# Kernel optimization log

Measured on AMD Instinct MI355X. Metric: run time of the kernel, lower is better.

## Reference

```python
import jax, jax.numpy as jnp
import numpy as np

H = 256        # hidden_dim
GD = 16        # genome_dim
GL = 16        # genome_len
L = 2          # n_layers
NH = 4         # n_heads
ED = 256       # embed_dim (of generated network)
CS = 256       # chunk_size (== H so chunk feedback into GRU is well-formed)
TOTAL = 4 * ED * ED + 4 * ED          # 263168
NCH = (TOTAL + CS - 1) // CS          # 1028 sequential GRU steps
B = 16


def setup_inputs() -> dict:
    key = jax.random.key(0)
    ks = iter(jax.random.split(key, 32))
    def p(shape, s=0.02):
        return jax.random.normal(next(ks), shape, jnp.float32) * s
    return dict(
        genome_seq=jax.random.normal(next(ks), (B, GL, GD), jnp.float32),
        embed_W=p((H, GD)), embed_b=jnp.zeros((H,), jnp.float32),
        qkv_W=p((L, 3 * H, H)), qkv_b=jnp.zeros((L, 3 * H), jnp.float32),
        attn_out_W=p((L, H, H)), attn_out_b=jnp.zeros((L, H), jnp.float32),
        ln1_g=jnp.ones((L, H), jnp.float32), ln1_b=jnp.zeros((L, H), jnp.float32),
        ln2_g=jnp.ones((L, H), jnp.float32), ln2_b=jnp.zeros((L, H), jnp.float32),
        ffn_W1=p((L, 4 * H, H)), ffn_b1=jnp.zeros((L, 4 * H), jnp.float32),
        ffn_W2=p((L, H, 4 * H)), ffn_b2=jnp.zeros((L, H), jnp.float32),
        gru_Wih=p((3 * H, H)), gru_Whh=p((3 * H, H)),
        gru_bih=jnp.zeros((3 * H,), jnp.float32), gru_bhh=jnp.zeros((3 * H,), jnp.float32),
        out_W=p((CS, H)), out_b=jnp.zeros((CS,), jnp.float32),
    )


def _ln(x, g, b, eps=1e-5):
    m = x.mean(-1, keepdims=True)
    v = ((x - m) ** 2).mean(-1, keepdims=True)
    return (x - m) / jnp.sqrt(v + eps) * g + b


def reference(genome_seq, embed_W, embed_b, qkv_W, qkv_b, attn_out_W, attn_out_b,
              ln1_g, ln1_b, ln2_g, ln2_b, ffn_W1, ffn_b1, ffn_W2, ffn_b2,
              gru_Wih, gru_Whh, gru_bih, gru_bhh, out_W, out_b):
    b = genome_seq.shape[0]
    dh = H // NH
    scale = 1.0 / np.sqrt(dh).astype(np.float32)

    h = genome_seq @ embed_W.T + embed_b                      # [B, S, H]
    # post-norm transformer encoder, relu FFN (PyTorch defaults, no dropout)
    for l in range(L):
        qkv = h @ qkv_W[l].T + qkv_b[l]                        # [B, S, 3H]
        q, k, v = jnp.split(qkv, 3, axis=-1)
        q = q.reshape(b, GL, NH, dh)
        k = k.reshape(b, GL, NH, dh)
        v = v.reshape(b, GL, NH, dh)
        scores = jnp.einsum('bshd,bthd->bhst', q, k) * scale
        attn = jax.nn.softmax(scores, axis=-1)
        o = jnp.einsum('bhst,bthd->bshd', attn, v).reshape(b, GL, H)
        h = _ln(h + o @ attn_out_W[l].T + attn_out_b[l], ln1_g[l], ln1_b[l])
        f = jax.nn.relu(h @ ffn_W1[l].T + ffn_b1[l]) @ ffn_W2[l].T + ffn_b2[l]
        h = _ln(h + f, ln2_g[l], ln2_b[l])

    latent = h.mean(axis=1)                                    # [B, H]

    # sequential chunk generation: 1 GRU step + Linear per chunk, fed back
    def step(carry, _):
        x, hid = carry
        gi = x @ gru_Wih.T + gru_bih
        gh = hid @ gru_Whh.T + gru_bhh
        ir, iz, inn = jnp.split(gi, 3, axis=-1)
        hr, hz, hn = jnp.split(gh, 3, axis=-1)
        r = jax.nn.sigmoid(ir + hr)
        z = jax.nn.sigmoid(iz + hz)
        n = jnp.tanh(inn + r * hn)
        hid = (1.0 - z) * n + z * hid
        chunk = hid @ out_W.T + out_b                          # [B, CS]
        return (chunk, hid), chunk

    h0 = jnp.zeros((b, H), latent.dtype)
    _, chunks = jax.lax.scan(step, (latent, h0), None, length=NCH)  # [NCH, B, CS]
    flat = jnp.moveaxis(chunks, 0, 1).reshape(b, NCH * CS)
    return flat[:, :TOTAL]
```

## Files before the change

kernel.cpp:

```cpp
#include <hip/hip_runtime.h>


typedef unsigned int uint_t;
typedef int v4i __attribute__((ext_vector_type(4)));

static constexpr size_t WS_HB   = 0;
static constexpr size_t WS_QKV  = 65536;
static constexpr size_t WS_AO   = 262144;
static constexpr size_t WS_F1   = 327680;
static constexpr size_t WS_LAT  = 589824;
static constexpr size_t WS_GI0  = 593920;
static constexpr size_t WS_CV   = 606208;
static constexpr size_t WS_MS   = 607232;
static constexpr size_t WS_M8   = 608256;
static constexpr size_t WS_HSEQ = 673792;

__device__ inline float sigf(float x){
    return __builtin_amdgcn_rcpf(1.0f + __builtin_amdgcn_exp2f(-1.442695041f*x));
}
__device__ inline float tanh_fast(float x){
    return 1.0f - 2.0f*__builtin_amdgcn_rcpf(1.0f + __builtin_amdgcn_exp2f(2.885390082f*x));
}


__global__ __launch_bounds__(256) void k_embed(const float* gs, const float* eW,
                                               const float* eb, float* ws){
    int bs = blockIdx.x;
    int i  = threadIdx.x;
    const float* g = gs + bs*16;
    float acc = eb[i];
#pragma unroll
    for(int d=0; d<16; ++d) acc += g[d]*eW[i*16+d];
    ws[WS_HB + (size_t)bs*256 + i] = acc;
}

__global__ __launch_bounds__(256) void k_qkv(const float* qkvW, const float* qkvb,
                                             float* ws, int l){
    __shared__ float hr[16][256];
    int b = blockIdx.x, jc = blockIdx.y;
    for(int idx=threadIdx.x; idx<4096; idx+=256)
        hr[idx>>8][idx&255] = ws[WS_HB + (size_t)(b*16+(idx>>8))*256 + (idx&255)];
    __syncthreads();
    int j = jc*256 + threadIdx.x;
    float bias = qkvb[l*768 + j];
    float acc[16];
#pragma unroll
    for(int s=0;s<16;++s) acc[s]=bias;
    const float* wr = qkvW + (size_t)(l*768 + j)*256;
    for(int k=0;k<256;k+=4){
        float4 w4 = *(const float4*)(wr+k);
#pragma unroll
        for(int s=0;s<16;++s)
            acc[s] += w4.x*hr[s][k] + w4.y*hr[s][k+1] + w4.z*hr[s][k+2] + w4.w*hr[s][k+3];
    }
    for(int s=0;s<16;++s) ws[WS_QKV + (size_t)(b*16+s)*768 + j] = acc[s];
}

__global__ __launch_bounds__(256) void k_attn(float* ws){
    __shared__ float ql[16][64], kl[16][64], vl[16][64], sc[16][16];
    int b = blockIdx.x>>2, hh = blockIdx.x&3;
    for(int idx=threadIdx.x; idx<1024; idx+=256){
        int s_=idx>>6, d=idx&63;
        const float* base = &ws[WS_QKV + (size_t)(b*16+s_)*768 + hh*64 + d];
        ql[s_][d]=base[0]; kl[s_][d]=base[256]; vl[s_][d]=base[512];
    }
    __syncthreads();
    int s = threadIdx.x>>4, t = threadIdx.x&15;
    float a=0.f;
#pragma unroll
    for(int d=0; d<64; ++d) a += ql[s][d]*kl[t][d];
    sc[s][t] = a*0.125f;
    __syncthreads();
    if(threadIdx.x<16){
        int r=threadIdx.x;
        float m=-1e30f;
#pragma unroll
        for(int tt=0;tt<16;++tt) m=fmaxf(m,sc[r][tt]);
        float e[16]; float sum=0.f;
#pragma unroll
        for(int tt=0;tt<16;++tt){ e[tt]=__expf(sc[r][tt]-m); sum+=e[tt]; }
        float inv=1.0f/sum;
#pragma unroll
        for(int tt=0;tt<16;++tt) sc[r][tt]=e[tt]*inv;
    }
    __syncthreads();
    int dg = (threadIdx.x&15)*4;
#pragma unroll
    for(int dd=0;dd<4;++dd){
        int d = dg+dd; float o=0.f;
#pragma unroll
        for(int tt=0;tt<16;++tt) o += sc[s][tt]*vl[tt][d];
        ws[WS_AO + (size_t)(b*16+s)*256 + hh*64 + d] = o;
    }
}

__global__ __launch_bounds__(256) void k_ao_ln(const float* aoW, const float* aob,
                                               const float* g1, const float* b1,
                                               float* ws, int l){
    __shared__ float ao[256]; __shared__ float red[256];
    int bs = blockIdx.x, i = threadIdx.x;
    ao[i] = ws[WS_AO + (size_t)bs*256 + i];
    __syncthreads();
    const float* wr = aoW + (size_t)(l*256+i)*256;
    float acc = aob[l*256+i];
    for(int k=0;k<256;k+=4){
        float4 w4 = *(const float4*)(wr+k);
        acc += w4.x*ao[k]+w4.y*ao[k+1]+w4.z*ao[k+2]+w4.w*ao[k+3];
    }
    float x = ws[WS_HB + (size_t)bs*256 + i] + acc;
    red[i]=x; __syncthreads();
    for(int off=128;off>0;off>>=1){ if(i<off) red[i]+=red[i+off]; __syncthreads(); }
    float m = red[0]*(1.0f/256.0f); __syncthreads();
    float d = x-m;
    red[i]=d*d; __syncthreads();
    for(int off=128;off>0;off>>=1){ if(i<off) red[i]+=red[i+off]; __syncthreads(); }
    float v = red[0]*(1.0f/256.0f);
    float y = d / sqrtf(v+1e-5f);
    ws[WS_HB + (size_t)bs*256 + i] = y*g1[l*256+i] + b1[l*256+i];
}

__global__ __launch_bounds__(256) void k_ffn1(const float* W1, const float* fb1,
                                              float* ws, int l){
    __shared__ float hr[16][256];
    int b = blockIdx.x, jc = blockIdx.y;
    for(int idx=threadIdx.x; idx<4096; idx+=256)
        hr[idx>>8][idx&255] = ws[WS_HB + (size_t)(b*16+(idx>>8))*256 + (idx&255)];
    __syncthreads();
    int j = jc*256 + threadIdx.x;
    float bias = fb1[l*1024+j];
    float acc[16];
#pragma unroll
    for(int s=0;s<16;++s) acc[s]=bias;
    const float* wr = W1 + (size_t)(l*1024+j)*256;
    for(int k=0;k<256;k+=4){
        float4 w4 = *(const float4*)(wr+k);
#pragma unroll
        for(int s=0;s<16;++s)
            acc[s] += w4.x*hr[s][k] + w4.y*hr[s][k+1] + w4.z*hr[s][k+2] + w4.w*hr[s][k+3];
    }
    for(int s=0;s<16;++s)
        ws[WS_F1 + (size_t)(b*16+s)*1024 + j] = fmaxf(acc[s],0.0f);
}

__global__ __launch_bounds__(256) void k_ffn2_ln(const float* W2, const float* fb2,
                                                 const float* g2, const float* b2v,
                                                 float* ws, int l){
    __shared__ float f1r[1024]; __shared__ float red[256];
    int bs = blockIdx.x, i = threadIdx.x;
    for(int idx=i; idx<1024; idx+=256) f1r[idx] = ws[WS_F1 + (size_t)bs*1024 + idx];
    __syncthreads();
    const float* wr = W2 + (size_t)(l*256+i)*1024;
    float acc = fb2[l*256+i];
    for(int k=0;k<1024;k+=4){
        float4 w4 = *(const float4*)(wr+k);
        acc += w4.x*f1r[k]+w4.y*f1r[k+1]+w4.z*f1r[k+2]+w4.w*f1r[k+3];
    }
    float x = ws[WS_HB + (size_t)bs*256 + i] + acc;
    red[i]=x; __syncthreads();
    for(int off=128;off>0;off>>=1){ if(i<off) red[i]+=red[i+off]; __syncthreads(); }
    float m = red[0]*(1.0f/256.0f); __syncthreads();
    float d = x-m;
    red[i]=d*d; __syncthreads();
    for(int off=128;off>0;off>>=1){ if(i<off) red[i]+=red[i+off]; __syncthreads(); }
    float v = red[0]*(1.0f/256.0f);
    float y = d / sqrtf(v+1e-5f);
    ws[WS_HB + (size_t)bs*256 + i] = y*g2[l*256+i] + b2v[l*256+i];
}

__global__ __launch_bounds__(256) void k_latent(float* ws){
    int b=blockIdx.x, i=threadIdx.x; float a=0.f;
#pragma unroll
    for(int s=0;s<16;++s) a += ws[WS_HB + (size_t)(b*16+s)*256 + i];
    ws[WS_LAT + (size_t)b*256 + i] = a*(1.0f/16.0f);
}


__global__ __launch_bounds__(768) void k_gi0(const float* Wih, const float* bih,
                                             float* ws){
    __shared__ float lat[256];
    int b=blockIdx.x, j=threadIdx.x;
    if(j<256) lat[j]=ws[WS_LAT + (size_t)b*256 + j];
    __syncthreads();
    const float* wr = Wih + (size_t)j*256;
    float acc = bih[j];
    for(int k=0;k<256;k+=4){
        float4 w4=*(const float4*)(wr+k);
        acc += w4.x*lat[k]+w4.y*lat[k+1]+w4.z*lat[k+2]+w4.w*lat[k+3];
    }
    ws[WS_GI0 + (size_t)b*768 + j] = acc;
}

__global__ __launch_bounds__(256) void k_prepm(const float* Wih, const float* Whh,
                                               const float* bih, const float* bhh,
                                               const float* outW, const float* outb,
                                               float* ws){
    __shared__ float wrow[256]; __shared__ float red[256];
    __shared__ signed char q8[256];
    int r=blockIdx.x, c=threadIdx.x;
    bool hasA = (r<768);
    wrow[c] = hasA ? Wih[(size_t)r*256+c] : 0.0f;
    __syncthreads();
    float m;
    if(hasA){
        float a=0.f;
        for(int k=0;k<256;++k) a += wrow[k]*outW[(size_t)k*256+c];
        if(r<512) a += Whh[(size_t)r*256+c];
        m=a;
    } else {
        m = Whh[(size_t)(r-256)*256+c];
    }
    red[c] = wrow[c]*outb[c];
    __syncthreads();
    for(int off=128;off>0;off>>=1){ if(c<off) red[c]+=red[c+off]; __syncthreads(); }
    if(c==0){
        float cv;
        if(r<512)       cv = red[0] + bih[r] + bhh[r];
        else if(r<768)  cv = red[0] + bih[r];
        else            cv = bhh[r-256];
        ws[WS_CV + r] = cv;
    }
    __syncthreads();
    red[c] = fabsf(m);
    __syncthreads();
    for(int off=128;off>0;off>>=1){ if(c<off) red[c]=fmaxf(red[c],red[c+off]); __syncthreads(); }
    float rowmax = red[0];
    float inv = rowmax>0.f ? 127.0f/rowmax : 0.0f;
    q8[c] = (signed char)__float2int_rn(m*inv);
    if(c==0) ws[WS_MS + r] = rowmax>0.f ? rowmax*(1.0f/(127.0f*127.0f)) : 0.0f;
    __syncthreads();
    if(c<64){
        uint_t u = ((uint_t)(unsigned char)q8[4*c  ])
                 | ((uint_t)(unsigned char)q8[4*c+1] << 8)
                 | ((uint_t)(unsigned char)q8[4*c+2] << 16)
                 | ((uint_t)(unsigned char)q8[4*c+3] << 24);
        ((uint_t*)ws)[WS_M8 + (size_t)r*64 + c] = u;
    }
}


__global__ __launch_bounds__(512,2) void k_chain(const float* bhh, float* ws){
    __shared__ alignas(16) signed char h8[2][256];
    int tid = threadIdx.x;
    int b   = blockIdx.x;
    int l   = tid & 63;
    int w   = tid >> 6;
    int col = l & 15;
    int grp = l >> 4;
    int g0  = w*32 + col;

    const uint_t* Mdw = (const uint_t*)ws + WS_M8;

    v4i wf[8][4];
    float C8[8], MS8[8];
#pragma unroll
    for(int s=0;s<4;++s){
#pragma unroll
        for(int half=0; half<2; ++half){
            int f = s*2 + half;
            int row = s*256 + w*32 + half*16 + col;
            const uint_t* src = Mdw + (size_t)row*64 + grp*4;
#pragma unroll
            for(int kt=0;kt<4;++kt)
                wf[f][kt] = *(const v4i*)(src + kt*16);
            C8[f]  = ws[WS_CV + row];
            MS8[f] = ws[WS_MS + row];
        }
    }

    const float* gi = ws + WS_GI0 + (size_t)b*768;
    int g1 = g0 + 16;
    float r0 = sigf(gi[g0]     + bhh[g0]);
    float z0 = sigf(gi[256+g0] + bhh[256+g0]);
    float n0 = tanh_fast(gi[512+g0] + r0*bhh[512+g0]);
    float hp0 = (1.0f-z0)*n0;
    float r1 = sigf(gi[g1]     + bhh[g1]);
    float z1 = sigf(gi[256+g1] + bhh[256+g1]);
    float n1 = tanh_fast(gi[512+g1] + r1*bhh[512+g1]);
    float hp1 = (1.0f-z1)*n1;

    float* hsp = ws + WS_HSEQ + (size_t)b*256;
    if(grp < 2){
        float v = grp ? hp1 : hp0;
        h8[0][w*32 + (l&31)] = (signed char)__float2int_rn(v*127.0f);
        hsp[w*32 + (l&31)] = v;
    }
    asm volatile("s_waitcnt lgkmcnt(0)" ::: "memory");
    __builtin_amdgcn_s_barrier();
    asm volatile("" ::: "memory");

    const v4i vzero = {0,0,0,0};
    int po = 0;
    for(int t=1; t<1028; ++t){
        hsp += 4096;
        v4i af[4];
#pragma unroll
        for(int kt=0;kt<4;++kt)
            af[kt] = *(const v4i*)&h8[po][kt*64 + grp*16];
        v4i acc[8];
#pragma unroll
        for(int f=0;f<8;++f){
            acc[f] = __builtin_amdgcn_mfma_i32_16x16x64_i8(af[0], wf[f][0], vzero, 0,0,0);
#pragma unroll
            for(int kt=1;kt<4;++kt)
                acc[f] = __builtin_amdgcn_mfma_i32_16x16x64_i8(af[kt], wf[f][kt], acc[f], 0,0,0);
        }
        float yr0 = MS8[0]*(float)acc[0][0] + C8[0];
        float yr1 = MS8[1]*(float)acc[1][0] + C8[1];
        float yz0 = MS8[2]*(float)acc[2][0] + C8[2];
        float yz1 = MS8[3]*(float)acc[3][0] + C8[3];
        float yn0 = MS8[4]*(float)acc[4][0] + C8[4];
        float yn1 = MS8[5]*(float)acc[5][0] + C8[5];
        float yh0 = MS8[6]*(float)acc[6][0] + C8[6];
        float yh1 = MS8[7]*(float)acc[7][0] + C8[7];
        float rr0 = sigf(yr0), rr1 = sigf(yr1);
        float zz0 = sigf(yz0), zz1 = sigf(yz1);
        float nn0 = tanh_fast(yn0 + rr0*yh0);
        float nn1 = tanh_fast(yn1 + rr1*yh1);
        hp0 = (1.0f-zz0)*nn0 + zz0*hp0;
        hp1 = (1.0f-zz1)*nn1 + zz1*hp1;
        if(grp < 2){
            float v = grp ? hp1 : hp0;
            h8[po^1][w*32 + (l&31)] = (signed char)__float2int_rn(v*127.0f);
            hsp[w*32 + (l&31)] = v;
        }
        asm volatile("s_waitcnt lgkmcnt(0)" ::: "memory");
        __builtin_amdgcn_s_barrier();
        asm volatile("" ::: "memory");
        po ^= 1;
    }
}

__global__ __launch_bounds__(256) void k_epi(const float* outW, const float* outb,
                                             const float* ws, float* out){
    __shared__ float ht[16][256];
    int t = blockIdx.x, j = threadIdx.x;
    for(int idx=j; idx<4096; idx+=256)
        ht[idx>>8][idx&255] = ws[WS_HSEQ + (size_t)t*4096 + idx];
    __syncthreads();
    const float* wr = outW + (size_t)j*256;
    float bias = outb[j];
    float acc[16];
#pragma unroll
    for(int bb=0;bb<16;++bb) acc[bb]=bias;
    for(int k=0;k<256;k+=4){
        float4 w4 = *(const float4*)(wr+k);
#pragma unroll
        for(int bb=0;bb<16;++bb)
            acc[bb] += w4.x*ht[bb][k]+w4.y*ht[bb][k+1]+w4.z*ht[bb][k+2]+w4.w*ht[bb][k+3];
    }
#pragma unroll
    for(int bb=0;bb<16;++bb)
        out[(size_t)bb*263168 + (size_t)t*256 + j] = acc[bb];
}


extern "C" void kernel_launch(void* const* d_in, const int* in_sizes, int n_in,
                              void* d_out, int out_size, void* d_ws, size_t ws_size,
                              hipStream_t stream){
    const float* gs   = (const float*)d_in[0];
    const float* eW   = (const float*)d_in[1];
    const float* eb   = (const float*)d_in[2];
    const float* qkvW = (const float*)d_in[3];
    const float* qkvb = (const float*)d_in[4];
    const float* aoW  = (const float*)d_in[5];
    const float* aob  = (const float*)d_in[6];
    const float* g1   = (const float*)d_in[7];
    const float* b1   = (const float*)d_in[8];
    const float* g2   = (const float*)d_in[9];
    const float* b2   = (const float*)d_in[10];
    const float* W1   = (const float*)d_in[11];
    const float* fb1  = (const float*)d_in[12];
    const float* W2   = (const float*)d_in[13];
    const float* fb2  = (const float*)d_in[14];
    const float* Wih  = (const float*)d_in[15];
    const float* Whh  = (const float*)d_in[16];
    const float* bih  = (const float*)d_in[17];
    const float* bhh  = (const float*)d_in[18];
    const float* outW = (const float*)d_in[19];
    const float* outb = (const float*)d_in[20];
    float* ws  = (float*)d_ws;
    float* out = (float*)d_out;

    k_embed<<<256,256,0,stream>>>(gs,eW,eb,ws);
    for(int l=0;l<2;++l){
        k_qkv    <<<dim3(16,3),256,0,stream>>>(qkvW,qkvb,ws,l);
        k_attn   <<<64,256,0,stream>>>(ws);
        k_ao_ln  <<<256,256,0,stream>>>(aoW,aob,g1,b1,ws,l);
        k_ffn1   <<<dim3(16,4),256,0,stream>>>(W1,fb1,ws,l);
        k_ffn2_ln<<<256,256,0,stream>>>(W2,fb2,g2,b2,ws,l);
    }
    k_latent<<<16,256,0,stream>>>(ws);
    k_gi0   <<<16,768,0,stream>>>(Wih,bih,ws);
    k_prepm <<<1024,256,0,stream>>>(Wih,Whh,bih,bhh,outW,outb,ws);
    k_chain <<<16,512,0,stream>>>(bhh,ws);
    k_epi   <<<1028,256,0,stream>>>(outW,outb,ws,out);
}
```

Before: 1.127 ms.

## Fuse transformer front-end, latent, gi0 and weight prep into one kernel

Replaces the twelve-plus small launches (embed, per-layer qkv/attn/ao_ln/ffn1/ffn2_ln, latent, gi0, prepm) with one 32-block kernel. Blocks 0-15 each run the whole encoder for one batch element, and blocks 16-31 do the fused-weight int8 quantization concurrently. The aim is to remove launch overhead and inter-kernel gaps, at the cost of far less parallelism per stage; each batch block now does all matmuls serially. The GRU chain kernel is also reworked so each lane computes a single hidden unit chosen by lane parity, cutting per-step elementwise gate work in half.

Result: slower. 2.302 ms (+104.4%).

```diff
diff --git a/kernel.cpp b/kernel.cpp
--- a/kernel.cpp
+++ b/kernel.cpp
@@ -8,7 +8,6 @@
 static constexpr size_t WS_QKV  = 65536;
 static constexpr size_t WS_AO   = 262144;
 static constexpr size_t WS_F1   = 327680;
-static constexpr size_t WS_LAT  = 589824;
 static constexpr size_t WS_GI0  = 593920;
 static constexpr size_t WS_CV   = 606208;
 static constexpr size_t WS_MS   = 607232;
@@ -23,217 +22,256 @@
 }
 
 
-__global__ __launch_bounds__(256) void k_embed(const float* gs, const float* eW,
-                                               const float* eb, float* ws){
-    int bs = blockIdx.x;
-    int i  = threadIdx.x;
-    const float* g = gs + bs*16;
-    float acc = eb[i];
-#pragma unroll
-    for(int d=0; d<16; ++d) acc += g[d]*eW[i*16+d];
-    ws[WS_HB + (size_t)bs*256 + i] = acc;
-}
-
-__global__ __launch_bounds__(256) void k_qkv(const float* qkvW, const float* qkvb,
-                                             float* ws, int l){
-    __shared__ float hr[16][256];
-    int b = blockIdx.x, jc = blockIdx.y;
-    for(int idx=threadIdx.x; idx<4096; idx+=256)
-        hr[idx>>8][idx&255] = ws[WS_HB + (size_t)(b*16+(idx>>8))*256 + (idx&255)];
+__global__ __launch_bounds__(512) void k_front(
+    const float* gs, const float* eW, const float* eb,
+    const float* qkvW, const float* qkvb,
+    const float* aoW, const float* aob,
+    const float* g1, const float* b1, const float* g2, const float* b2v,
+    const float* W1, const float* fb1, const float* W2, const float* fb2,
+    const float* Wih, const float* bih,
+    const float* Whh, const float* bhh,
+    const float* outW, const float* outb,
+    float* ws)
+{
+    __shared__ float s_a[16][256];
+    __shared__ float s_sc[16][16];
+    __shared__ float s_p[2][4];
+    __shared__ float s_lat[256];
+    int tid = threadIdx.x;
+
+    if(blockIdx.x >= 16){
+        int pb = blockIdx.x - 16;
+        float* wrow = &s_a[0][0];
+        float* redf = &s_a[2][0];
+        signed char* q8 = (signed char*)&s_a[4][0];
+        int rh = tid >> 8, c = tid & 255;
+        int wv = tid >> 6;
+        for(int it=0; it<32; ++it){
+            int r = pb*64 + it*2 + rh;
+            bool hasA = (r < 768);
+            wrow[rh*256+c] = hasA ? Wih[(size_t)r*256+c] : 0.0f;
+            __syncthreads();
+            float m;
+            if(hasA){
+                float a = 0.f;
+                for(int k=0;k<256;++k) a += wrow[rh*256+k]*outW[(size_t)k*256+c];
+                if(r<512) a += Whh[(size_t)r*256+c];
+                m = a;
+            } else {
+                m = Whh[(size_t)(r-256)*256+c];
+            }
+            float pv = wrow[rh*256+c]*outb[c];
+            for(int mk=1; mk<64; mk<<=1) pv += __shfl_xor(pv, mk);
+            if((tid&63)==0) redf[wv] = pv;
+            __syncthreads();
+            if(c==0){
+                float cv_sum = redf[rh*4+0]+redf[rh*4+1]+redf[rh*4+2]+redf[rh*4+3];
+                float cv;
+                if(r<512)       cv = cv_sum + bih[r] + bhh[r];
+                else if(r<768)  cv = cv_sum + bih[r];
+                else            cv = bhh[r-256];
+                ws[WS_CV + r] = cv;
+            }
+            float av = fabsf(m);
+            for(int mk=1; mk<64; mk<<=1) av = fmaxf(av, __shfl_xor(av, mk));
+            if((tid&63)==0) redf[16+wv] = av;
+            __syncthreads();
+            float rowmax = fmaxf(fmaxf(redf[16+rh*4],redf[17+rh*4]),
+                                 fmaxf(redf[18+rh*4],redf[19+rh*4]));
+            float inv = rowmax>0.f ? 127.0f/rowmax : 0.0f;
+            q8[rh*256+c] = (signed char)__float2int_rn(m*inv);
+            if(c==0) ws[WS_MS + r] = rowmax>0.f ? rowmax*(1.0f/(127.0f*127.0f)) : 0.0f;
+            __syncthreads();
+            if(c<64){
+                uint_t u = ((uint_t)(unsigned char)q8[rh*256+4*c  ])
+                         | ((uint_t)(unsigned char)q8[rh*256+4*c+1] << 8)
+                         | ((uint_t)(unsigned char)q8[rh*256+4*c+2] << 16)
+                         | ((uint_t)(unsigned char)q8[rh*256+4*c+3] << 24);
+                ((uint_t*)ws)[WS_M8 + (size_t)r*64 + c] = u;
+            }
+            __syncthreads();
+        }
+        return;
+    }
+
+    int b = blockIdx.x;
+    int rh = tid >> 8, ci = tid & 255;
+    int wv4 = (tid >> 6) & 3;
+
+    for(int u=tid; u<4096; u+=512){
+        int s=u>>8, i=u&255;
+        const float* g = gs + (b*16+s)*16;
+        float acc = eb[i];
+#pragma unroll
+        for(int d=0;d<16;++d) acc += g[d]*eW[i*16+d];
+        ws[WS_HB + (size_t)(b*16+s)*256 + i] = acc;
+    }
     __syncthreads();
-    int j = jc*256 + threadIdx.x;
-    float bias = qkvb[l*768 + j];
-    float acc[16];
-#pragma unroll
-    for(int s=0;s<16;++s) acc[s]=bias;
-    const float* wr = qkvW + (size_t)(l*768 + j)*256;
-    for(int k=0;k<256;k+=4){
-        float4 w4 = *(const float4*)(wr+k);
-#pragma unroll
-        for(int s=0;s<16;++s)
-            acc[s] += w4.x*hr[s][k] + w4.y*hr[s][k+1] + w4.z*hr[s][k+2] + w4.w*hr[s][k+3];
-    }
-    for(int s=0;s<16;++s) ws[WS_QKV + (size_t)(b*16+s)*768 + j] = acc[s];
-}
-
-__global__ __launch_bounds__(256) void k_attn(float* ws){
-    __shared__ float ql[16][64], kl[16][64], vl[16][64], sc[16][16];
-    int b = blockIdx.x>>2, hh = blockIdx.x&3;
-    for(int idx=threadIdx.x; idx<1024; idx+=256){
-        int s_=idx>>6, d=idx&63;
-        const float* base = &ws[WS_QKV + (size_t)(b*16+s_)*768 + hh*64 + d];
-        ql[s_][d]=base[0]; kl[s_][d]=base[256]; vl[s_][d]=base[512];
+
+    for(int l=0;l<2;++l){
+        for(int u=tid; u<4096; u+=512)
+            s_a[u>>8][u&255] = ws[WS_HB + (size_t)(b*16+(u>>8))*256 + (u&255)];
+        __syncthreads();
+        for(int j=tid; j<768; j+=512){
+            const float* wr = qkvW + (size_t)(l*768+j)*256;
+            float bias = qkvb[l*768+j];
+            float acc[16];
+#pragma unroll
+            for(int s=0;s<16;++s) acc[s]=bias;
+            for(int k=0;k<256;k+=4){
+                float4 w4 = *(const float4*)(wr+k);
+#pragma unroll
+                for(int s=0;s<16;++s){
+                    float4 h4 = *(const float4*)&s_a[s][k];
+                    acc[s] += w4.x*h4.x + w4.y*h4.y + w4.z*h4.z + w4.w*h4.w;
+                }
+            }
+            for(int s=0;s<16;++s) ws[WS_QKV + (size_t)(b*16+s)*768 + j] = acc[s];
+        }
+        __syncthreads();
+
+        for(int hh=0; hh<4; ++hh){
+            for(int u=tid; u<1024; u+=512){
+                int s=u>>6, d=u&63;
+                const float* base = &ws[WS_QKV + (size_t)(b*16+s)*768 + hh*64 + d];
+                s_a[s][d]     = base[0];
+                s_a[s][64+d]  = base[256];
+                s_a[s][128+d] = base[512];
+            }
+            __syncthreads();
+            if(tid<256){
+                int s=tid>>4, t=tid&15;
+                float a=0.f;
+#pragma unroll
+                for(int d=0;d<64;++d) a += s_a[s][d]*s_a[t][64+d];
+                s_sc[s][t] = a*0.125f;
+            }
+            __syncthreads();
+            if(tid<16){
+                int r=tid;
+                float m=-1e30f;
+#pragma unroll
+                for(int tt=0;tt<16;++tt) m=fmaxf(m,s_sc[r][tt]);
+                float e[16]; float sum=0.f;
+#pragma unroll
+                for(int tt=0;tt<16;++tt){ e[tt]=__expf(s_sc[r][tt]-m); sum+=e[tt]; }
+                float inv=1.0f/sum;
+#pragma unroll
+                for(int tt=0;tt<16;++tt) s_sc[r][tt]=e[tt]*inv;
+            }
+            __syncthreads();
+            for(int u=tid; u<1024; u+=512){
+                int s=u>>6, d=u&63;
+                float o=0.f;
+#pragma unroll
+                for(int t2=0;t2<16;++t2) o += s_sc[s][t2]*s_a[t2][128+d];
+                ws[WS_AO + (size_t)(b*16+s)*256 + hh*64 + d] = o;
+            }
+            __syncthreads();
+        }
+
+        for(int u=tid; u<4096; u+=512)
+            s_a[u>>8][u&255] = ws[WS_AO + (size_t)(b*16+(u>>8))*256 + (u&255)];
+        __syncthreads();
+        for(int it=0; it<8; ++it){
+            int s = it*2 + rh;
+            const float* wr = aoW + (size_t)(l*256+ci)*256;
+            float acc = aob[l*256+ci];
+            for(int k=0;k<256;k+=4){
+                float4 w4 = *(const float4*)(wr+k);
+                float4 h4 = *(const float4*)&s_a[s][k];
+                acc += w4.x*h4.x + w4.y*h4.y + w4.z*h4.z + w4.w*h4.w;
+            }
+            float x = ws[WS_HB + (size_t)(b*16+s)*256 + ci] + acc;
+            float pv = x;
+            for(int mk=1;mk<64;mk<<=1) pv += __shfl_xor(pv, mk);
+            if((tid&63)==0) s_p[rh][wv4] = pv;
+            __syncthreads();
+            float mean = (s_p[rh][0]+s_p[rh][1]+s_p[rh][2]+s_p[rh][3])*(1.0f/256.0f);
+            float d = x - mean;
+            float qv = d*d;
+            for(int mk=1;mk<64;mk<<=1) qv += __shfl_xor(qv, mk);
+            __syncthreads();
+            if((tid&63)==0) s_p[rh][wv4] = qv;
+            __syncthreads();
+            float var = (s_p[rh][0]+s_p[rh][1]+s_p[rh][2]+s_p[rh][3])*(1.0f/256.0f);
+            float y = d / sqrtf(var+1e-5f);
+            ws[WS_HB + (size_t)(b*16+s)*256 + ci] = y*g1[l*256+ci] + b1[l*256+ci];
+            __syncthreads();
+        }
+
+        for(int u=tid; u<4096; u+=512)
+            s_a[u>>8][u&255] = ws[WS_HB + (size_t)(b*16+(u>>8))*256 + (u&255)];
+        __syncthreads();
+        for(int j=tid; j<1024; j+=512){
+            const float* wr = W1 + (size_t)(l*1024+j)*256;
+            float bias = fb1[l*1024+j];
+            float acc[16];
+#pragma unroll
+            for(int s=0;s<16;++s) acc[s]=bias;
+            for(int k=0;k<256;k+=4){
+                float4 w4 = *(const float4*)(wr+k);
+#pragma unroll
+                for(int s=0;s<16;++s){
+                    float4 h4 = *(const float4*)&s_a[s][k];
+                    acc[s] += w4.x*h4.x + w4.y*h4.y + w4.z*h4.z + w4.w*h4.w;
+                }
+            }
+            for(int s=0;s<16;++s)
+                ws[WS_F1 + (size_t)(b*16+s)*1024 + j] = fmaxf(acc[s],0.0f);
+        }
+        __syncthreads();
+
+        {
+            float* f1p = &s_a[0][0];
+            for(int it=0; it<8; ++it){
+                for(int u=tid; u<2048; u+=512)
+                    f1p[u] = ws[WS_F1 + (size_t)(b*16 + it*2 + (u>>10))*1024 + (u&1023)];
+                __syncthreads();
+                int s = it*2 + rh;
+                const float* wr = W2 + (size_t)(l*256+ci)*1024;
+                float acc = fb2[l*256+ci];
+                for(int k=0;k<1024;k+=4){
+                    float4 w4 = *(const float4*)(wr+k);
+                    float4 h4 = *(const float4*)(f1p + rh*1024 + k);
+                    acc += w4.x*h4.x + w4.y*h4.y + w4.z*h4.z + w4.w*h4.w;
+                }
+                float x = ws[WS_HB + (size_t)(b*16+s)*256 + ci] + acc;
+                float pv = x;
+                for(int mk=1;mk<64;mk<<=1) pv += __shfl_xor(pv, mk);
+                if((tid&63)==0) s_p[rh][wv4] = pv;
+                __syncthreads();
+                float mean = (s_p[rh][0]+s_p[rh][1]+s_p[rh][2]+s_p[rh][3])*(1.0f/256.0f);
+                float d = x - mean;
+                float qv = d*d;
+                for(int mk=1;mk<64;mk<<=1) qv += __shfl_xor(qv, mk);
+                __syncthreads();
+                if((tid&63)==0) s_p[rh][wv4] = qv;
+                __syncthreads();
+                float var = (s_p[rh][0]+s_p[rh][1]+s_p[rh][2]+s_p[rh][3])*(1.0f/256.0f);
+                float y = d / sqrtf(var+1e-5f);
+                ws[WS_HB + (size_t)(b*16+s)*256 + ci] = y*g2[l*256+ci] + b2v[l*256+ci];
+                __syncthreads();
+            }
+        }
+    }
+
+    if(tid<256){
+        float a=0.f;
+#pragma unroll
+        for(int s=0;s<16;++s) a += ws[WS_HB + (size_t)(b*16+s)*256 + tid];
+        s_lat[tid] = a*(1.0f/16.0f);
     }
     __syncthreads();
-    int s = threadIdx.x>>4, t = threadIdx.x&15;
-    float a=0.f;
-#pragma unroll
-    for(int d=0; d<64; ++d) a += ql[s][d]*kl[t][d];
-    sc[s][t] = a*0.125f;
-    __syncthreads();
-    if(threadIdx.x<16){
-        int r=threadIdx.x;
-        float m=-1e30f;
-#pragma unroll
-        for(int tt=0;tt<16;++tt) m=fmaxf(m,sc[r][tt]);
-        float e[16]; float sum=0.f;
-#pragma unroll
-        for(int tt=0;tt<16;++tt){ e[tt]=__expf(sc[r][tt]-m); sum+=e[tt]; }
-        float inv=1.0f/sum;
-#pragma unroll
-        for(int tt=0;tt<16;++tt) sc[r][tt]=e[tt]*inv;
-    }
-    __syncthreads();
-    int dg = (threadIdx.x&15)*4;
-#pragma unroll
-    for(int dd=0;dd<4;++dd){
-        int d = dg+dd; float o=0.f;
-#pragma unroll
-        for(int tt=0;tt<16;++tt) o += sc[s][tt]*vl[tt][d];
-        ws[WS_AO + (size_t)(b*16+s)*256 + hh*64 + d] = o;
-    }
-}
-
-__global__ __launch_bounds__(256) void k_ao_ln(const float* aoW, const float* aob,
-                                               const float* g1, const float* b1,
-                                               float* ws, int l){
-    __shared__ float ao[256]; __shared__ float red[256];
-    int bs = blockIdx.x, i = threadIdx.x;
-    ao[i] = ws[WS_AO + (size_t)bs*256 + i];
-    __syncthreads();
-    const float* wr = aoW + (size_t)(l*256+i)*256;
-    float acc = aob[l*256+i];
-    for(int k=0;k<256;k+=4){
-        float4 w4 = *(const float4*)(wr+k);
-        acc += w4.x*ao[k]+w4.y*ao[k+1]+w4.z*ao[k+2]+w4.w*ao[k+3];
-    }
-    float x = ws[WS_HB + (size_t)bs*256 + i] + acc;
-    red[i]=x; __syncthreads();
-    for(int off=128;off>0;off>>=1){ if(i<off) red[i]+=red[i+off]; __syncthreads(); }
-    float m = red[0]*(1.0f/256.0f); __syncthreads();
-    float d = x-m;
-    red[i]=d*d; __syncthreads();
-    for(int off=128;off>0;off>>=1){ if(i<off) red[i]+=red[i+off]; __syncthreads(); }
-    float v = red[0]*(1.0f/256.0f);
-    float y = d / sqrtf(v+1e-5f);
-    ws[WS_HB + (size_t)bs*256 + i] = y*g1[l*256+i] + b1[l*256+i];
-}
-
-__global__ __launch_bounds__(256) void k_ffn1(const float* W1, const float* fb1,
-                                              float* ws, int l){
-    __shared__ float hr[16][256];
-    int b = blockIdx.x, jc = blockIdx.y;
-    for(int idx=threadIdx.x; idx<4096; idx+=256)
-        hr[idx>>8][idx&255] = ws[WS_HB + (size_t)(b*16+(idx>>8))*256 + (idx&255)];
-    __syncthreads();
-    int j = jc*256 + threadIdx.x;
-    float bias = fb1[l*1024+j];
-    float acc[16];
-#pragma unroll
-    for(int s=0;s<16;++s) acc[s]=bias;
-    const float* wr = W1 + (size_t)(l*1024+j)*256;
-    for(int k=0;k<256;k+=4){
-        float4 w4 = *(const float4*)(wr+k);
-#pragma unroll
-        for(int s=0;s<16;++s)
-            acc[s] += w4.x*hr[s][k] + w4.y*hr[s][k+1] + w4.z*hr[s][k+2] + w4.w*hr[s][k+3];
-    }
-    for(int s=0;s<16;++s)
-        ws[WS_F1 + (size_t)(b*16+s)*1024 + j] = fmaxf(acc[s],0.0f);
-}
-
-__global__ __launch_bounds__(256) void k_ffn2_ln(const float* W2, const float* fb2,
-                                                 const float* g2, const float* b2v,
-                                                 float* ws, int l){
-    __shared__ float f1r[1024]; __shared__ float red[256];
-    int bs = blockIdx.x, i = threadIdx.x;
-    for(int idx=i; idx<1024; idx+=256) f1r[idx] = ws[WS_F1 + (size_t)bs*1024 + idx];
-    __syncthreads();
-    const float* wr = W2 + (size_t)(l*256+i)*1024;
-    float acc = fb2[l*256+i];
-    for(int k=0;k<1024;k+=4){
-        float4 w4 = *(const float4*)(wr+k);
-        acc += w4.x*f1r[k]+w4.y*f1r[k+1]+w4.z*f1r[k+2]+w4.w*f1r[k+3];
-    }
-    float x = ws[WS_HB + (size_t)bs*256 + i] + acc;
-    red[i]=x; __syncthreads();
-    for(int off=128;off>0;off>>=1){ if(i<off) red[i]+=red[i+off]; __syncthreads(); }
-    float m = red[0]*(1.0f/256.0f); __syncthreads();
-    float d = x-m;
-    red[i]=d*d; __syncthreads();
-    for(int off=128;off>0;off>>=1){ if(i<off) red[i]+=red[i+off]; __syncthreads(); }
-    float v = red[0]*(1.0f/256.0f);
-    float y = d / sqrtf(v+1e-5f);
-    ws[WS_HB + (size_t)bs*256 + i] = y*g2[l*256+i] + b2v[l*256+i];
-}
-
-__global__ __launch_bounds__(256) void k_latent(float* ws){
-    int b=blockIdx.x, i=threadIdx.x; float a=0.f;
-#pragma unroll
-    for(int s=0;s<16;++s) a += ws[WS_HB + (size_t)(b*16+s)*256 + i];
-    ws[WS_LAT + (size_t)b*256 + i] = a*(1.0f/16.0f);
-}
-
-
-__global__ __launch_bounds__(768) void k_gi0(const float* Wih, const float* bih,
-                                             float* ws){
-    __shared__ float lat[256];
-    int b=blockIdx.x, j=threadIdx.x;
-    if(j<256) lat[j]=ws[WS_LAT + (size_t)b*256 + j];
-    __syncthreads();
-    const float* wr = Wih + (size_t)j*256;
-    float acc = bih[j];
-    for(int k=0;k<256;k+=4){
-        float4 w4=*(const float4*)(wr+k);
-        acc += w4.x*lat[k]+w4.y*lat[k+1]+w4.z*lat[k+2]+w4.w*lat[k+3];
-    }
-    ws[WS_GI0 + (size_t)b*768 + j] = acc;
-}
-
-__global__ __launch_bounds__(256) void k_prepm(const float* Wih, const float* Whh,
-                                               const float* bih, const float* bhh,
-                                               const float* outW, const float* outb,
-                                               float* ws){
-    __shared__ float wrow[256]; __shared__ float red[256];
-    __shared__ signed char q8[256];
-    int r=blockIdx.x, c=threadIdx.x;
-    bool hasA = (r<768);
-    wrow[c] = hasA ? Wih[(size_t)r*256+c] : 0.0f;
-    __syncthreads();
-    float m;
-    if(hasA){
-        float a=0.f;
-        for(int k=0;k<256;++k) a += wrow[k]*outW[(size_t)k*256+c];
-        if(r<512) a += Whh[(size_t)r*256+c];
-        m=a;
-    } else {
-        m = Whh[(size_t)(r-256)*256+c];
-    }
-    red[c] = wrow[c]*outb[c];
-    __syncthreads();
-    for(int off=128;off>0;off>>=1){ if(c<off) red[c]+=red[c+off]; __syncthreads(); }
-    if(c==0){
-        float cv;
-        if(r<512)       cv = red[0] + bih[r] + bhh[r];
-        else if(r<768)  cv = red[0] + bih[r];
-        else            cv = bhh[r-256];
-        ws[WS_CV + r] = cv;
-    }
-    __syncthreads();
-    red[c] = fabsf(m);
-    __syncthreads();
-    for(int off=128;off>0;off>>=1){ if(c<off) red[c]=fmaxf(red[c],red[c+off]); __syncthreads(); }
-    float rowmax = red[0];
-    float inv = rowmax>0.f ? 127.0f/rowmax : 0.0f;
-    q8[c] = (signed char)__float2int_rn(m*inv);
-    if(c==0) ws[WS_MS + r] = rowmax>0.f ? rowmax*(1.0f/(127.0f*127.0f)) : 0.0f;
-    __syncthreads();
-    if(c<64){
-        uint_t u = ((uint_t)(unsigned char)q8[4*c  ])
-                 | ((uint_t)(unsigned char)q8[4*c+1] << 8)
-                 | ((uint_t)(unsigned char)q8[4*c+2] << 16)
-                 | ((uint_t)(unsigned char)q8[4*c+3] << 24);
-        ((uint_t*)ws)[WS_M8 + (size_t)r*64 + c] = u;
+    for(int j=tid; j<768; j+=512){
+        const float* wr = Wih + (size_t)j*256;
+        float acc = bih[j];
+        for(int k=0;k<256;k+=4){
+            float4 w4 = *(const float4*)(wr+k);
+            float4 l4 = *(const float4*)&s_lat[k];
+            acc += w4.x*l4.x + w4.y*l4.y + w4.z*l4.z + w4.w*l4.w;
+        }
+        ws[WS_GI0 + (size_t)b*768 + j] = acc;
     }
 }
 
@@ -246,12 +284,12 @@
     int w   = tid >> 6;
     int col = l & 15;
     int grp = l >> 4;
-    int g0  = w*32 + col;
+    int par = grp & 1;
+    int ge  = w*32 + par*16 + col;
 
     const uint_t* Mdw = (const uint_t*)ws + WS_M8;
 
     v4i wf[8][4];
-    float C8[8], MS8[8];
 #pragma unroll
     for(int s=0;s<4;++s){
 #pragma unroll
@@ -262,27 +300,26 @@
 #pragma unroll
             for(int kt=0;kt<4;++kt)
                 wf[f][kt] = *(const v4i*)(src + kt*16);
-            C8[f]  = ws[WS_CV + row];
-            MS8[f] = ws[WS_MS + row];
-        }
+        }
+    }
+    float Cs[4], MSs[4];
+#pragma unroll
+    for(int s=0;s<4;++s){
+        int row = s*256 + ge;
+        Cs[s]  = ws[WS_CV + row];
+        MSs[s] = ws[WS_MS + row];
     }
 
     const float* gi = ws + WS_GI0 + (size_t)b*768;
-    int g1 = g0 + 16;
-    float r0 = sigf(gi[g0]     + bhh[g0]);
-    float z0 = sigf(gi[256+g0] + bhh[256+g0]);
-    float n0 = tanh_fast(gi[512+g0] + r0*bhh[512+g0]);
-    float hp0 = (1.0f-z0)*n0;
-    float r1 = sigf(gi[g1]     + bhh[g1]);
-    float z1 = sigf(gi[256+g1] + bhh[256+g1]);
-    float n1 = tanh_fast(gi[512+g1] + r1*bhh[512+g1]);
-    float hp1 = (1.0f-z1)*n1;
+    float r0 = sigf(gi[ge]     + bhh[ge]);
+    float z0 = sigf(gi[256+ge] + bhh[256+ge]);
+    float n0 = tanh_fast(gi[512+ge] + r0*bhh[512+ge]);
+    float hp = (1.0f-z0)*n0;
 
     float* hsp = ws + WS_HSEQ + (size_t)b*256;
     if(grp < 2){
-        float v = grp ? hp1 : hp0;
-        h8[0][w*32 + (l&31)] = (signed char)__float2int_rn(v*127.0f);
-        hsp[w*32 + (l&31)] = v;
+        h8[0][w*32 + (l&31)] = (signed char)__float2int_rn(hp*127.0f);
+        hsp[w*32 + (l&31)] = hp;
     }
     asm volatile("s_waitcnt lgkmcnt(0)" ::: "memory");
     __builtin_amdgcn_s_barrier();
@@ -304,24 +341,21 @@
             for(int kt=1;kt<4;++kt)
                 acc[f] = __builtin_amdgcn_mfma_i32_16x16x64_i8(af[kt], wf[f][kt], acc[f], 0,0,0);
         }
-        float yr0 = MS8[0]*(float)acc[0][0] + C8[0];
-        float yr1 = MS8[1]*(float)acc[1][0] + C8[1];
-        float yz0 = MS8[2]*(float)acc[2][0] + C8[2];
-        float yz1 = MS8[3]*(float)acc[3][0] + C8[3];
-        float yn0 = MS8[4]*(float)acc[4][0] + C8[4];
-        float yn1 = MS8[5]*(float)acc[5][0] + C8[5];
-        float yh0 = MS8[6]*(float)acc[6][0] + C8[6];
-        float yh1 = MS8[7]*(float)acc[7][0] + C8[7];
-        float rr0 = sigf(yr0), rr1 = sigf(yr1);
-        float zz0 = sigf(yz0), zz1 = sigf(yz1);
-        float nn0 = tanh_fast(yn0 + rr0*yh0);
-        float nn1 = tanh_fast(yn1 + rr1*yh1);
-        hp0 = (1.0f-zz0)*nn0 + zz0*hp0;
-        hp1 = (1.0f-zz1)*nn1 + zz1*hp1;
+        int a_r = par ? acc[1][0] : acc[0][0];
+        int a_z = par ? acc[3][0] : acc[2][0];
+        int a_n = par ? acc[5][0] : acc[4][0];
+        int a_h = par ? acc[7][0] : acc[6][0];
+        float yr = MSs[0]*(float)a_r + Cs[0];
+        float yz = MSs[1]*(float)a_z + Cs[1];
+        float yn = MSs[2]*(float)a_n + Cs[2];
+        float yh = MSs[3]*(float)a_h + Cs[3];
+        float rr = sigf(yr);
+        float zz = sigf(yz);
+        float nn = tanh_fast(yn + rr*yh);
+        hp = (1.0f-zz)*nn + zz*hp;
         if(grp < 2){
-            float v = grp ? hp1 : hp0;
-            h8[po^1][w*32 + (l&31)] = (signed char)__float2int_rn(v*127.0f);
-            hsp[w*32 + (l&31)] = v;
+            h8[po^1][w*32 + (l&31)] = (signed char)__float2int_rn(hp*127.0f);
+            hsp[w*32 + (l&31)] = hp;
         }
         asm volatile("s_waitcnt lgkmcnt(0)" ::: "memory");
         __builtin_amdgcn_s_barrier();
@@ -381,17 +415,8 @@
     float* ws  = (float*)d_ws;
     float* out = (float*)d_out;
 
-    k_embed<<<256,256,0,stream>>>(gs,eW,eb,ws);
-    for(int l=0;l<2;++l){
-        k_qkv    <<<dim3(16,3),256,0,stream>>>(qkvW,qkvb,ws,l);
-        k_attn   <<<64,256,0,stream>>>(ws);
-        k_ao_ln  <<<256,256,0,stream>>>(aoW,aob,g1,b1,ws,l);
-        k_ffn1   <<<dim3(16,4),256,0,stream>>>(W1,fb1,ws,l);
-        k_ffn2_ln<<<256,256,0,stream>>>(W2,fb2,g2,b2,ws,l);
-    }
-    k_latent<<<16,256,0,stream>>>(ws);
-    k_gi0   <<<16,768,0,stream>>>(Wih,bih,ws);
-    k_prepm <<<1024,256,0,stream>>>(Wih,Whh,bih,bhh,outW,outb,ws);
-    k_chain <<<16,512,0,stream>>>(bhh,ws);
-    k_epi   <<<1028,256,0,stream>>>(outW,outb,ws,out);
-}
+    k_front<<<32,512,0,stream>>>(gs,eW,eb,qkvW,qkvb,aoW,aob,g1,b1,g2,b2,
+                                 W1,fb1,W2,fb2,Wih,bih,Whh,bhh,outW,outb,ws);
+    k_chain<<<16,512,0,stream>>>(bhh,ws);
+    k_epi  <<<1028,256,0,stream>>>(outW,outb,ws,out);
+}
```
